# Kernel tuning notes

Measured on AMD Instinct MI355X. Metric: run time of the kernel, lower is better.

Reference implementation:

```python
import jax, jax.numpy as jnp
import numpy as np

NUM_HEADS = 8


def setup_inputs() -> dict:
    key = jax.random.key(0)
    ks = jax.random.split(key, 5)
    B, N, D = 2, 2048, 512
    scale = 1.0 / np.sqrt(D)  # xavier-ish init for stability
    return {
        "x": jax.random.normal(ks[0], (B, N, D), dtype=jnp.float32),
        "Wq": jax.random.normal(ks[1], (D, D), dtype=jnp.float32) * scale,
        "Wk": jax.random.normal(ks[2], (D, D), dtype=jnp.float32) * scale,
        "Wv": jax.random.normal(ks[3], (D, D), dtype=jnp.float32) * scale,
        "Wo": jax.random.normal(ks[4], (D, D), dtype=jnp.float32) * scale,
        "log_c": jnp.zeros((), dtype=jnp.float32),
        "log_beta": jnp.zeros((), dtype=jnp.float32),
    }


def reference(x, Wq, Wk, Wv, Wo, log_c, log_beta):
    B, N, D = x.shape
    H = NUM_HEADS
    dh = D // H

    # torch nn.Linear: y = x @ W.T
    def proj(W):
        return (x @ W.T).reshape(B, N, H, dh).transpose(0, 2, 1, 3)  # [B,H,N,dh]

    q, k, v = proj(Wq), proj(Wk), proj(Wv)

    c = jax.nn.softplus(log_c)
    beta = jax.nn.softplus(log_beta) + 0.5

    q_nsq = jnp.sum(q * q, axis=-1)  # [B,H,N]
    k_nsq = jnp.sum(k * k, axis=-1)  # [B,H,N]
    qk = jnp.einsum("bhnd,bhmd->bhnm", q, k)  # [B,H,N,N]

    diff_sq = jnp.maximum(q_nsq[..., :, None] - 2.0 * qk + k_nsq[..., None, :], 0.0)
    hyp_factor = jnp.sqrt(1.0 + c * (q_nsq[..., :, None] + k_nsq[..., None, :]))
    dist = jnp.sqrt(diff_sq + 1e-8) * hyp_factor
    scores = -beta * dist

    # causal mask (original: causal = mask is not None)
    causal = jnp.tril(jnp.ones((N, N), dtype=bool))
    scores = jnp.where(causal, scores, -jnp.inf)

    p = jax.nn.softmax(scores, axis=-1)
    out = jnp.einsum("bhnm,bhmd->bhnd", p, v)  # [B,H,N,dh]
    out = out.transpose(0, 2, 1, 3).reshape(B, N, D)
    return out @ Wo.T
```

## Files before the change

kernel.cpp:

```cpp
#include <hip/hip_runtime.h>
#include <math.h>

#define BB   2
#define NN   2048
#define DDIM 512
#define HH   8
#define DH   64
#define MTOT (BB*NN)
#define EE   (BB*HH*NN*DH)
#define CPB  144
#define NSLOT (BB*HH*CPB)

typedef __attribute__((ext_vector_type(8))) short bf16x8;
typedef __attribute__((ext_vector_type(4))) float f32x4;

__device__ __forceinline__ float softplus_f(float x) {
    return x > 20.f ? x : log1pf(expf(x));
}
__device__ __forceinline__ unsigned short f2bf(float x) {
    union { float f; unsigned u; } v; v.f = x;
    unsigned r = v.u + 0x7fffu + ((v.u >> 16) & 1u);
    return (unsigned short)(r >> 16);
}
__device__ __forceinline__ float bf2f(unsigned short h) {
    union { unsigned u; float f; } v; v.u = ((unsigned)h) << 16; return v.f;
}
__device__ __forceinline__ void split4(float4 v, ushort4& h, ushort4& l) {
    h.x = f2bf(v.x); l.x = f2bf(v.x - bf2f(h.x));
    h.y = f2bf(v.y); l.y = f2bf(v.y - bf2f(h.y));
    h.z = f2bf(v.z); l.z = f2bf(v.z - bf2f(h.z));
    h.w = f2bf(v.w); l.w = f2bf(v.w - bf2f(h.w));
}

__global__ __launch_bounds__(256, 3)
void mm_proj(const float* __restrict__ Xf,
             const float* __restrict__ W0, const float* __restrict__ W1,
             const float* __restrict__ W2,
             unsigned short* __restrict__ Qhi, unsigned short* __restrict__ Qlo,
             unsigned short* __restrict__ Khi, unsigned short* __restrict__ Klo,
             unsigned short* __restrict__ Vt,
             float* __restrict__ QN, float* __restrict__ KN)
{
    const int mode = blockIdx.z;
    const float* W = (mode == 1) ? W1 : ((mode == 2) ? W2 : W0);
    const int m0 = blockIdx.x * 64, n0 = blockIdx.y * 128;

    __shared__ unsigned short Ah_s[4 * 64 * 8];
    __shared__ unsigned short Al_s[4 * 64 * 8];
    __shared__ unsigned short Bh_s[4 * 128 * 8];
    __shared__ unsigned short Bl_s[4 * 128 * 8];

    const int tid  = threadIdx.x;
    const int lane = tid & 63, lx = lane & 15, q4 = lane >> 4;
    const int w = tid >> 6, wm = w & 1, wn = w >> 1;
    const int rowA = tid & 63, kqA = tid >> 6;
    const int rowB = tid & 127, kbB = tid >> 7;

    f32x4 acc[2][4];
    #pragma unroll
    for (int mt = 0; mt < 2; ++mt)
        #pragma unroll
        for (int nt = 0; nt < 4; ++nt)
            acc[mt][nt] = (f32x4){0.f, 0.f, 0.f, 0.f};

    const int am = m0 + rowA;
    const size_t brow = (size_t)(n0 + rowB) * DDIM;

    float4 fa0, fa1, fb0, fb1, fb2, fb3;
    {
        const float* ap = Xf + (size_t)am * DDIM + kqA * 8;
        fa0 = *(const float4*)(ap);
        fa1 = *(const float4*)(ap + 4);
        const int eb = kbB * 8;
        fb0 = *(const float4*)(W + brow + eb);
        fb1 = *(const float4*)(W + brow + eb + 4);
        fb2 = *(const float4*)(W + brow + eb + 16);
        fb3 = *(const float4*)(W + brow + eb + 20);
    }

    for (int k0 = 0; k0 < DDIM; k0 += 32) {
        __syncthreads();
        {
            ushort4 h0, l0, h1, l1;
            split4(fa0, h0, l0); split4(fa1, h1, l1);
            const int off = (kqA << 9) + (rowA << 3);
            *(ushort4*)&Ah_s[off]     = h0;  *(ushort4*)&Ah_s[off + 4] = h1;
            *(ushort4*)&Al_s[off]     = l0;  *(ushort4*)&Al_s[off + 4] = l1;
            split4(fb0, h0, l0); split4(fb1, h1, l1);
            const int offb = (kbB << 10) + (rowB << 3);
            *(ushort4*)&Bh_s[offb]     = h0;  *(ushort4*)&Bh_s[offb + 4] = h1;
            *(ushort4*)&Bl_s[offb]     = l0;  *(ushort4*)&Bl_s[offb + 4] = l1;
            split4(fb2, h0, l0); split4(fb3, h1, l1);
            const int offb2 = ((kbB + 2) << 10) + (rowB << 3);
            *(ushort4*)&Bh_s[offb2]     = h0;  *(ushort4*)&Bh_s[offb2 + 4] = h1;
            *(ushort4*)&Bl_s[offb2]     = l0;  *(ushort4*)&Bl_s[offb2 + 4] = l1;
        }
        __syncthreads();

        if (k0 + 32 < DDIM) {
            const float* ap = Xf + (size_t)am * DDIM + k0 + 32 + kqA * 8;
            fa0 = *(const float4*)(ap);
            fa1 = *(const float4*)(ap + 4);
            const int eb = k0 + 32 + kbB * 8;
            fb0 = *(const float4*)(W + brow + eb);
            fb1 = *(const float4*)(W + brow + eb + 4);
            fb2 = *(const float4*)(W + brow + eb + 16);
            fb3 = *(const float4*)(W + brow + eb + 20);
        }

        bf16x8 fah[2], fal[2], fbh[4], fbl[4];
        #pragma unroll
        for (int mt = 0; mt < 2; ++mt) {
            const int off = (q4 << 9) + ((wm * 32 + mt * 16 + lx) << 3);
            fah[mt] = *(const bf16x8*)&Ah_s[off];
            fal[mt] = *(const bf16x8*)&Al_s[off];
        }
        #pragma unroll
        for (int nt = 0; nt < 4; ++nt) {
            const int off = (q4 << 10) + ((wn * 64 + nt * 16 + lx) << 3);
            fbh[nt] = *(const bf16x8*)&Bh_s[off];
            fbl[nt] = *(const bf16x8*)&Bl_s[off];
        }
        #pragma unroll
        for (int mt = 0; mt < 2; ++mt)
            #pragma unroll
            for (int nt = 0; nt < 4; ++nt) {
                acc[mt][nt] = __builtin_amdgcn_mfma_f32_16x16x32_bf16(fah[mt], fbh[nt], acc[mt][nt], 0, 0, 0);
                acc[mt][nt] = __builtin_amdgcn_mfma_f32_16x16x32_bf16(fah[mt], fbl[nt], acc[mt][nt], 0, 0, 0);
                acc[mt][nt] = __builtin_amdgcn_mfma_f32_16x16x32_bf16(fal[mt], fbh[nt], acc[mt][nt], 0, 0, 0);
            }
    }

    if (mode == 0 || mode == 1) {
        float* Np = (mode == 0) ? QN : KN;
        const int head = (n0 + wn * 64) >> 6;
        #pragma unroll
        for (int mt = 0; mt < 2; ++mt)
            #pragma unroll
            for (int r = 0; r < 4; ++r) {
                float s = 0.f;
                #pragma unroll
                for (int nt = 0; nt < 4; ++nt) s = fmaf(acc[mt][nt][r], acc[mt][nt][r], s);
                s += __shfl_xor(s, 1);
                s += __shfl_xor(s, 2);
                s += __shfl_xor(s, 4);
                s += __shfl_xor(s, 8);
                if (lx == 0) {
                    const int m = m0 + wm * 32 + mt * 16 + q4 * 4 + r;
                    Np[(size_t)((m >> 11) * HH + head) * NN + (m & 2047)] = s;
                }
            }
    }

    if (mode == 2) {
        #pragma unroll
        for (int mt = 0; mt < 2; ++mt) {
            const int mb = m0 + wm * 32 + mt * 16 + q4 * 4;
            const int b = mb >> 11, nb = mb & 2047;
            #pragma unroll
            for (int nt = 0; nt < 4; ++nt) {
                const int j = n0 + wn * 64 + nt * 16 + lx;
                ushort4 pv = make_ushort4(f2bf(acc[mt][nt][0]), f2bf(acc[mt][nt][1]),
                                          f2bf(acc[mt][nt][2]), f2bf(acc[mt][nt][3]));
                *(ushort4*)(Vt + ((size_t)(b * HH + (j >> 6)) * 64 + (j & 63)) * NN + nb) = pv;
            }
        }
    } else {
        #pragma unroll
        for (int mt = 0; mt < 2; ++mt) {
            #pragma unroll
            for (int r = 0; r < 4; ++r) {
                const int m = m0 + wm * 32 + mt * 16 + q4 * 4 + r;
                const int b = m >> 11, n2 = m & 2047;
                #pragma unroll
                for (int nt = 0; nt < 4; ++nt) {
                    const int j = n0 + wn * 64 + nt * 16 + lx;
                    const float v = acc[mt][nt][r];
                    const size_t idx = (((size_t)(b * HH + (j >> 6)) * NN + n2) << 6) + (j & 63);
                    const unsigned short h = f2bf(v);
                    const unsigned short l = f2bf(v - bf2f(h));
                    if (mode == 0) { Qhi[idx] = h; Qlo[idx] = l; }
                    else           { Khi[idx] = h; Klo[idx] = l; }
                }
            }
        }
    }
}

__global__ __launch_bounds__(256, 4)
void mm_out(const unsigned short* __restrict__ AO, const float* __restrict__ Wo,
            float* __restrict__ Outp)
{
    const int m0 = blockIdx.x * 64, n0 = blockIdx.y * 64;

    __shared__ unsigned short Ah_s[4 * 64 * 8];
    __shared__ unsigned short Bh_s[4 * 64 * 8];

    const int tid  = threadIdx.x;
    const int lane = tid & 63, lx = lane & 15, q4 = lane >> 4;
    const int w = tid >> 6, wm = w & 1, wn = w >> 1;
    const int rowA = tid & 63, kqA = tid >> 6;

    f32x4 acc[2][2];
    #pragma unroll
    for (int mt = 0; mt < 2; ++mt)
        #pragma unroll
        for (int nt = 0; nt < 2; ++nt)
            acc[mt][nt] = (f32x4){0.f, 0.f, 0.f, 0.f};

    const int am = m0 + rowA;
    const int ab = am >> 11, an = am & 2047;
    const size_t brow = (size_t)(n0 + rowA) * DDIM;

    uint4 rah; float4 fb0, fb1;
    {
        const int e = kqA * 8;
        rah = *(const uint4*)(AO + (((size_t)(ab * HH + (e >> 6)) * NN + an) << 6) + (e & 63));
        fb0 = *(const float4*)(Wo + brow + e);
        fb1 = *(const float4*)(Wo + brow + e + 4);
    }

    for (int k0 = 0; k0 < DDIM; k0 += 32) {
        __syncthreads();
        {
            const int off = (kqA << 9) + (rowA << 3);
            *(uint4*)&Ah_s[off] = rah;
            ushort4 h0 = make_ushort4(f2bf(fb0.x), f2bf(fb0.y), f2bf(fb0.z), f2bf(fb0.w));
            ushort4 h1 = make_ushort4(f2bf(fb1.x), f2bf(fb1.y), f2bf(fb1.z), f2bf(fb1.w));
            *(ushort4*)&Bh_s[off]     = h0;
            *(ushort4*)&Bh_s[off + 4] = h1;
        }
        __syncthreads();

        if (k0 + 32 < DDIM) {
            const int e = k0 + 32 + kqA * 8;
            rah = *(const uint4*)(AO + (((size_t)(ab * HH + (e >> 6)) * NN + an) << 6) + (e & 63));
            fb0 = *(const float4*)(Wo + brow + e);
            fb1 = *(const float4*)(Wo + brow + e + 4);
        }

        bf16x8 fah[2], fbh[2];
        #pragma unroll
        for (int mt = 0; mt < 2; ++mt)
            fah[mt] = *(const bf16x8*)&Ah_s[(q4 << 9) + ((wm * 32 + mt * 16 + lx) << 3)];
        #pragma unroll
        for (int nt = 0; nt < 2; ++nt)
            fbh[nt] = *(const bf16x8*)&Bh_s[(q4 << 9) + ((wn * 32 + nt * 16 + lx) << 3)];
        #pragma unroll
        for (int mt = 0; mt < 2; ++mt)
            #pragma unroll
            for (int nt = 0; nt < 2; ++nt)
                acc[mt][nt] = __builtin_amdgcn_mfma_f32_16x16x32_bf16(fah[mt], fbh[nt], acc[mt][nt], 0, 0, 0);
    }

    #pragma unroll
    for (int mt = 0; mt < 2; ++mt)
        #pragma unroll
        for (int r = 0; r < 4; ++r) {
            const int m = m0 + wm * 32 + mt * 16 + q4 * 4 + r;
            #pragma unroll
            for (int nt = 0; nt < 2; ++nt)
                Outp[(size_t)m * DDIM + n0 + wn * 32 + nt * 16 + lx] = acc[mt][nt][r];
        }
}

__global__ __launch_bounds__(256, 4)
void attn_mfma(const unsigned short* __restrict__ Qhi, const unsigned short* __restrict__ Qlo,
               const unsigned short* __restrict__ Khi, const unsigned short* __restrict__ Klo,
               const unsigned short* __restrict__ Vt,
               const float* __restrict__ QN, const float* __restrict__ KN,
               const float* __restrict__ pLC, const float* __restrict__ pLB,
               float* __restrict__ Opart, float* __restrict__ Mp, float* __restrict__ Lp)
{
    __shared__ unsigned short Kh_s[8 * 64 * 8];
    __shared__ unsigned short Kl_s[8 * 64 * 8];
    __shared__ unsigned short Vt_s[8 * 64 * 8];
    __shared__ unsigned short P_s [8 * 64 * 8];
    __shared__ __align__(16) float kn_s[64];
    __shared__ float qn_s[64];

    const int idx = blockIdx.x;
    const int g   = (idx >= 112) ? 7 : (idx >= 84) ? 6 : (idx >= 60) ? 5 :
                    (idx >= 40) ? 4 : (idx >= 24) ? 3 : (idx >= 12) ? 2 :
                    (idx >= 4)  ? 1 : 0;
    const int rem = idx - 2 * g * (g + 1);
    const int C   = g + 1;
    const int qt  = g * 4 + rem / C;
    const int c0  = rem % C;
    const int bh  = blockIdx.y;
    const int nk  = qt + 1;
    const int kt0  = (c0 * nk) / C;
    const int kend = ((c0 + 1) * nk) / C;

    const int tid  = threadIdx.x;
    const int w    = tid >> 6;
    const int lane = tid & 63;
    const int lx   = lane & 15;
    const int q4   = lane >> 4;
    const int qrl  = w * 16 + lx;

    const float hc    = softplus_f(pLC[0]);
    const float betaL = (softplus_f(pLB[0]) + 0.5f) * 1.44269504f;

    const size_t base = ((size_t)bh * NN) << 6;

    const unsigned short* qrh = Qhi + base + ((size_t)(qt * 64 + qrl) << 6) + q4 * 8;
    const unsigned short* qrl_p = Qlo + base + ((size_t)(qt * 64 + qrl) << 6) + q4 * 8;
    const bf16x8 qh0 = *(const bf16x8*)(qrh);
    const bf16x8 qh1 = *(const bf16x8*)(qrh + 32);
    const bf16x8 ql0 = *(const bf16x8*)(qrl_p);
    const bf16x8 ql1 = *(const bf16x8*)(qrl_p + 32);

    if (tid < 64) qn_s[tid] = QN[(size_t)bh * NN + qt * 64 + tid];

    f32x4 Oacc[4];
    #pragma unroll
    for (int t = 0; t < 4; ++t) Oacc[t] = (f32x4){0.f, 0.f, 0.f, 0.f};
    float m_st = -INFINITY, l_st = 0.f;

    const int sc = tid >> 6, sr = tid & 63;

    uint4 pKh0, pKh1, pKl0, pKl1, pVt0, pVt1; float pkn = 0.f;
    {
        const unsigned short* kh = Khi + base + ((size_t)(kt0 * 64 + sr) << 6) + sc * 8;
        const unsigned short* kl = Klo + base + ((size_t)(kt0 * 64 + sr) << 6) + sc * 8;
        const unsigned short* vt = Vt  + base + (size_t)sr * NN + kt0 * 64 + sc * 8;
        pKh0 = *(const uint4*)(kh);  pKh1 = *(const uint4*)(kh + 32);
        pKl0 = *(const uint4*)(kl);  pKl1 = *(const uint4*)(kl + 32);
        pVt0 = *(const uint4*)(vt);  pVt1 = *(const uint4*)(vt + 32);
        if (tid < 64) pkn = KN[(size_t)bh * NN + kt0 * 64 + tid];
    }

    __syncthreads();
    const float qn = qn_s[qrl];

    for (int kt = kt0; kt < kend; ++kt) {
        const int soff = (sc << 9) + (sr << 3);
        *(uint4*)&Kh_s[soff]            = pKh0;
        *(uint4*)&Kh_s[soff + (4 << 9)] = pKh1;
        *(uint4*)&Kl_s[soff]            = pKl0;
        *(uint4*)&Kl_s[soff + (4 << 9)] = pKl1;
        *(uint4*)&Vt_s[soff]            = pVt0;
        *(uint4*)&Vt_s[soff + (4 << 9)] = pVt1;
        if (tid < 64) kn_s[tid] = pkn;
        __syncthreads();

        if (kt + 1 < kend) {
            const unsigned short* kh = Khi + base + ((size_t)((kt + 1) * 64 + sr) << 6) + sc * 8;
            const unsigned short* kl = Klo + base + ((size_t)((kt + 1) * 64 + sr) << 6) + sc * 8;
            const unsigned short* vt = Vt  + base + (size_t)sr * NN + (kt + 1) * 64 + sc * 8;
            pKh0 = *(const uint4*)(kh);  pKh1 = *(const uint4*)(kh + 32);
            pKl0 = *(const uint4*)(kl);  pKl1 = *(const uint4*)(kl + 32);
            pVt0 = *(const uint4*)(vt);  pVt1 = *(const uint4*)(vt + 32);
            if (tid < 64) pkn = KN[(size_t)bh * NN + (kt + 1) * 64 + tid];
        }

        f32x4 S[4];
        #pragma unroll
        for (int t = 0; t < 4; ++t) {
            f32x4 acc = (f32x4){0.f, 0.f, 0.f, 0.f};
            #pragma unroll
            for (int c2 = 0; c2 < 2; ++c2) {
                const int off = ((c2 * 4 + q4) << 9) + ((t * 16 + lx) << 3);
                const bf16x8 kh = *(const bf16x8*)&Kh_s[off];
                const bf16x8 kl = *(const bf16x8*)&Kl_s[off];
                const bf16x8 qh = c2 ? qh1 : qh0;
                const bf16x8 ql = c2 ? ql1 : ql0;
                acc = __builtin_amdgcn_mfma_f32_16x16x32_bf16(kh, qh, acc, 0, 0, 0);
                acc = __builtin_amdgcn_mfma_f32_16x16x32_bf16(kh, ql, acc, 0, 0, 0);
                acc = __builtin_amdgcn_mfma_f32_16x16x32_bf16(kl, qh, acc, 0, 0, 0);
            }
            S[t] = acc;
        }

        const bool diag = (kt == qt);
        float mloc = -INFINITY;
        #pragma unroll
        for (int t = 0; t < 4; ++t) {
            float kn4[4];
            *(float4*)kn4 = *(const float4*)&kn_s[t * 16 + q4 * 4];
            #pragma unroll
            for (int r = 0; r < 4; ++r) {
                const float sumn = qn + kn4[r];
                float diff = fmaxf(fmaf(-2.f, S[t][r], sumn), 0.f);
                float s = -betaL * sqrtf(fmaf(hc, sumn, 1.f) * (diff + 1e-8f));
                if (diag && (t * 16 + q4 * 4 + r) > qrl) s = -INFINITY;
                S[t][r] = s;
                mloc = fmaxf(mloc, s);
            }
        }
        mloc = fmaxf(mloc, __shfl_xor(mloc, 16));
        mloc = fmaxf(mloc, __shfl_xor(mloc, 32));
        const float mn = fmaxf(m_st, mloc);
        const float al = exp2f(m_st - mn);
        m_st = mn;

        float rs = 0.f;
        #pragma unroll
        for (int t = 0; t < 4; ++t) {
            const float p0 = exp2f(S[t][0] - mn);
            const float p1 = exp2f(S[t][1] - mn);
            const float p2 = exp2f(S[t][2] - mn);
            const float p3 = exp2f(S[t][3] - mn);
            rs += (p0 + p1) + (p2 + p3);
            ushort4 pk = make_ushort4(f2bf(p0), f2bf(p1), f2bf(p2), f2bf(p3));
            *(ushort4*)&P_s[((2 * t + (q4 >> 1)) << 9) + (qrl << 3) + ((q4 & 1) << 2)] = pk;
        }
        rs += __shfl_xor(rs, 16);
        rs += __shfl_xor(rs, 32);
        l_st = l_st * al + rs;
        #pragma unroll
        for (int t = 0; t < 4; ++t) {
            Oacc[t][0] *= al; Oacc[t][1] *= al;
            Oacc[t][2] *= al; Oacc[t][3] *= al;
        }

        __builtin_amdgcn_wave_barrier();

        #pragma unroll
        for (int c2 = 0; c2 < 2; ++c2) {
            const bf16x8 pb = *(const bf16x8*)&P_s[((c2 * 4 + q4) << 9) + (qrl << 3)];
            #pragma unroll
            for (int t2 = 0; t2 < 4; ++t2) {
                const bf16x8 va = *(const bf16x8*)&Vt_s[((c2 * 4 + q4) << 9) + ((t2 * 16 + lx) << 3)];
                Oacc[t2] = __builtin_amdgcn_mfma_f32_16x16x32_bf16(va, pb, Oacc[t2], 0, 0, 0);
            }
        }
        __syncthreads();
    }

    const int slot = bh * CPB + idx;
    float* op = Opart + ((size_t)slot << 12);
    #pragma unroll
    for (int t2 = 0; t2 < 4; ++t2)
        *(f32x4*)&op[qrl * 64 + t2 * 16 + q4 * 4] = Oacc[t2];
    if (q4 == 0) {
        Mp[slot * 64 + qrl] = m_st;
        Lp[slot * 64 + qrl] = l_st;
    }
}

__global__ __launch_bounds__(256)
void attn_combine(const float* __restrict__ Opart, const float* __restrict__ Mp,
                  const float* __restrict__ Lp, unsigned short* __restrict__ AO)
{
    const int bh = blockIdx.x >> 5, qt = blockIdx.x & 31;
    const int g = qt >> 2, C = g + 1;
    const int first = 2 * g * (g + 1) + (qt & 3) * C;
    const int row = threadIdx.x >> 2, qd = threadIdx.x & 3;
    const int slot0 = bh * CPB + first;

    float m = -INFINITY;
    for (int c = 0; c < C; ++c) m = fmaxf(m, Mp[(slot0 + c) * 64 + row]);
    float L = 0.f;
    float o[16];
    #pragma unroll
    for (int j = 0; j < 16; ++j) o[j] = 0.f;

    for (int c = 0; c < C; ++c) {
        const float wgt = exp2f(Mp[(slot0 + c) * 64 + row] - m);
        L += wgt * Lp[(slot0 + c) * 64 + row];
        const float* op = Opart + (((size_t)(slot0 + c)) << 12) + row * 64 + qd * 16;
        #pragma unroll
        for (int j4 = 0; j4 < 4; ++j4) {
            float4 v = *(const float4*)(op + j4 * 4);
            o[j4*4+0] = fmaf(wgt, v.x, o[j4*4+0]);
            o[j4*4+1] = fmaf(wgt, v.y, o[j4*4+1]);
            o[j4*4+2] = fmaf(wgt, v.z, o[j4*4+2]);
            o[j4*4+3] = fmaf(wgt, v.w, o[j4*4+3]);
        }
    }

    const float inv = 1.f / L;
    const size_t obase = (((size_t)bh * NN + qt * 64 + row) << 6) + qd * 16;
    union { unsigned short u[8]; uint4 v; } h2[2];
    #pragma unroll
    for (int j = 0; j < 16; ++j)
        h2[j >> 3].u[j & 7] = f2bf(o[j] * inv);
    *(uint4*)(AO + obase)     = h2[0].v;
    *(uint4*)(AO + obase + 8) = h2[1].v;
}

extern "C" void kernel_launch(void* const* d_in, const int* in_sizes, int n_in,
                              void* d_out, int out_size, void* d_ws, size_t ws_size,
                              hipStream_t stream)
{
    const float* x        = (const float*)d_in[0];
    const float* Wq       = (const float*)d_in[1];
    const float* Wk       = (const float*)d_in[2];
    const float* Wv       = (const float*)d_in[3];
    const float* Wo       = (const float*)d_in[4];
    const float* log_c    = (const float*)d_in[5];
    const float* log_beta = (const float*)d_in[6];
    float* out = (float*)d_out;

    unsigned short* p = (unsigned short*)d_ws;
    unsigned short* Qhi = p;            p += EE;
    unsigned short* Qlo = p;            p += EE;
    unsigned short* Khi = p;            p += EE;
    unsigned short* Klo = p;            p += EE;
    unsigned short* Vtr = p;            p += EE;
    unsigned short* AO  = p;            p += EE;
    float* QN    = (float*)p;
    float* KN    = QN + (size_t)BB * HH * NN;
    float* Opart = KN + (size_t)BB * HH * NN;
    float* Mp    = Opart + (size_t)NSLOT * 64 * 64;
    float* Lp    = Mp + (size_t)NSLOT * 64;

    mm_proj<<<dim3(MTOT / 64, DDIM / 128, 3), 256, 0, stream>>>(
        x, Wq, Wk, Wv, Qhi, Qlo, Khi, Klo, Vtr, QN, KN);
    attn_mfma<<<dim3(CPB, 16), 256, 0, stream>>>(Qhi, Qlo, Khi, Klo, Vtr, QN, KN,
                                                 log_c, log_beta, Opart, Mp, Lp);
    attn_combine<<<dim3(512), 256, 0, stream>>>(Opart, Mp, Lp, AO);
    mm_out<<<dim3(MTOT / 64, DDIM / 64), 256, 0, stream>>>(AO, Wo, out);
}
```

Before: 190.5 us.

## Pre-split weights to bf16, drop V split-precision MFMAs, store partials as bf16

Adds a split_w kernel that converts Wq/Wk/Wv into bf16 hi/lo pairs and Wo into bf16 once per call, so the GEMM kernels stop re-splitting fp32 weights in every block. The V projection (mode 2) now uses a single bf16 MFMA instead of three-term split precision. Attention partial outputs are written and read as bf16 rather than fp32, halving combine traffic. Conversions use hardware packed bf16 intrinsics. This adds an extra launch and lowers V and partial-output precision.

```diff
diff --git a/kernel.cpp b/kernel.cpp
--- a/kernel.cpp
+++ b/kernel.cpp
@@ -1,4 +1,5 @@
 #include <hip/hip_runtime.h>
+#include <hip/hip_bf16.h>
 #include <math.h>
 
 #define BB   2
@@ -8,6 +9,7 @@
 #define DH   64
 #define MTOT (BB*NN)
 #define EE   (BB*HH*NN*DH)
+#define WN   (DDIM*DDIM)
 #define CPB  144
 #define NSLOT (BB*HH*CPB)
 
@@ -31,18 +33,45 @@
     h.z = f2bf(v.z); l.z = f2bf(v.z - bf2f(h.z));
     h.w = f2bf(v.w); l.w = f2bf(v.w - bf2f(h.w));
 }
+__device__ __forceinline__ ushort4 pk4(float a, float b, float c, float d) {
+    union { __hip_bfloat162 b2[2]; ushort4 u4; } u;
+    u.b2[0] = __float22bfloat162_rn(make_float2(a, b));
+    u.b2[1] = __float22bfloat162_rn(make_float2(c, d));
+    return u.u4;
+}
+
+__global__ __launch_bounds__(256)
+void split_w(const float* __restrict__ Wq, const float* __restrict__ Wk,
+             const float* __restrict__ Wv, const float* __restrict__ Wo,
+             unsigned short* __restrict__ Whi, unsigned short* __restrict__ Wlo,
+             unsigned short* __restrict__ Wob)
+{
+    const int i = blockIdx.x * 256 + threadIdx.x;
+    const int y = blockIdx.y;
+    if (y < 3) {
+        const float* src = (y == 0) ? Wq : ((y == 1) ? Wk : Wv);
+        float4 v = *(const float4*)(src + 4 * (size_t)i);
+        ushort4 h, l;
+        split4(v, h, l);
+        *(ushort4*)(Whi + (size_t)y * WN + 4 * (size_t)i) = h;
+        *(ushort4*)(Wlo + (size_t)y * WN + 4 * (size_t)i) = l;
+    } else {
+        float4 v = *(const float4*)(Wo + 4 * (size_t)i);
+        *(ushort4*)(Wob + 4 * (size_t)i) = pk4(v.x, v.y, v.z, v.w);
+    }
+}
 
 __global__ __launch_bounds__(256, 3)
 void mm_proj(const float* __restrict__ Xf,
-             const float* __restrict__ W0, const float* __restrict__ W1,
-             const float* __restrict__ W2,
+             const unsigned short* __restrict__ Whi, const unsigned short* __restrict__ Wlo,
              unsigned short* __restrict__ Qhi, unsigned short* __restrict__ Qlo,
              unsigned short* __restrict__ Khi, unsigned short* __restrict__ Klo,
              unsigned short* __restrict__ Vt,
              float* __restrict__ QN, float* __restrict__ KN)
 {
     const int mode = blockIdx.z;
-    const float* W = (mode == 1) ? W1 : ((mode == 2) ? W2 : W0);
+    const unsigned short* Wh = Whi + (size_t)mode * WN;
+    const unsigned short* Wl = Wlo + (size_t)mode * WN;
     const int m0 = blockIdx.x * 64, n0 = blockIdx.y * 128;
 
     __shared__ unsigned short Ah_s[4 * 64 * 8];
@@ -66,16 +95,19 @@
     const int am = m0 + rowA;
     const size_t brow = (size_t)(n0 + rowB) * DDIM;
 
-    float4 fa0, fa1, fb0, fb1, fb2, fb3;
+    float4 fa0, fa1;
+    uint4 rbh0, rbh1, rbl0, rbl1;
     {
         const float* ap = Xf + (size_t)am * DDIM + kqA * 8;
         fa0 = *(const float4*)(ap);
         fa1 = *(const float4*)(ap + 4);
         const int eb = kbB * 8;
-        fb0 = *(const float4*)(W + brow + eb);
-        fb1 = *(const float4*)(W + brow + eb + 4);
-        fb2 = *(const float4*)(W + brow + eb + 16);
-        fb3 = *(const float4*)(W + brow + eb + 20);
+        rbh0 = *(const uint4*)(Wh + brow + eb);
+        rbh1 = *(const uint4*)(Wh + brow + eb + 16);
+        if (mode != 2) {
+            rbl0 = *(const uint4*)(Wl + brow + eb);
+            rbl1 = *(const uint4*)(Wl + brow + eb + 16);
+        }
     }
 
     for (int k0 = 0; k0 < DDIM; k0 += 32) {
@@ -85,15 +117,17 @@
             split4(fa0, h0, l0); split4(fa1, h1, l1);
             const int off = (kqA << 9) + (rowA << 3);
             *(ushort4*)&Ah_s[off]     = h0;  *(ushort4*)&Ah_s[off + 4] = h1;
-            *(ushort4*)&Al_s[off]     = l0;  *(ushort4*)&Al_s[off + 4] = l1;
-            split4(fb0, h0, l0); split4(fb1, h1, l1);
-            const int offb = (kbB << 10) + (rowB << 3);
-            *(ushort4*)&Bh_s[offb]     = h0;  *(ushort4*)&Bh_s[offb + 4] = h1;
-            *(ushort4*)&Bl_s[offb]     = l0;  *(ushort4*)&Bl_s[offb + 4] = l1;
-            split4(fb2, h0, l0); split4(fb3, h1, l1);
+            if (mode != 2) {
+                *(ushort4*)&Al_s[off]     = l0;  *(ushort4*)&Al_s[off + 4] = l1;
+            }
+            const int offb  = (kbB << 10) + (rowB << 3);
             const int offb2 = ((kbB + 2) << 10) + (rowB << 3);
-            *(ushort4*)&Bh_s[offb2]     = h0;  *(ushort4*)&Bh_s[offb2 + 4] = h1;
-            *(ushort4*)&Bl_s[offb2]     = l0;  *(ushort4*)&Bl_s[offb2 + 4] = l1;
+            *(uint4*)&Bh_s[offb]  = rbh0;
+            *(uint4*)&Bh_s[offb2] = rbh1;
+            if (mode != 2) {
+                *(uint4*)&Bl_s[offb]  = rbl0;
+                *(uint4*)&Bl_s[offb2] = rbl1;
+            }
         }
         __syncthreads();
 
@@ -102,10 +136,12 @@
             fa0 = *(const float4*)(ap);
             fa1 = *(const float4*)(ap + 4);
             const int eb = k0 + 32 + kbB * 8;
-            fb0 = *(const float4*)(W + brow + eb);
-            fb1 = *(const float4*)(W + brow + eb + 4);
-            fb2 = *(const float4*)(W + brow + eb + 16);
-            fb3 = *(const float4*)(W + brow + eb + 20);
+            rbh0 = *(const uint4*)(Wh + brow + eb);
+            rbh1 = *(const uint4*)(Wh + brow + eb + 16);
+            if (mode != 2) {
+                rbl0 = *(const uint4*)(Wl + brow + eb);
+                rbl1 = *(const uint4*)(Wl + brow + eb + 16);
+            }
         }
 
         bf16x8 fah[2], fal[2], fbh[4], fbl[4];
@@ -113,21 +149,23 @@
         for (int mt = 0; mt < 2; ++mt) {
             const int off = (q4 << 9) + ((wm * 32 + mt * 16 + lx) << 3);
             fah[mt] = *(const bf16x8*)&Ah_s[off];
-            fal[mt] = *(const bf16x8*)&Al_s[off];
+            if (mode != 2) fal[mt] = *(const bf16x8*)&Al_s[off];
         }
         #pragma unroll
         for (int nt = 0; nt < 4; ++nt) {
             const int off = (q4 << 10) + ((wn * 64 + nt * 16 + lx) << 3);
             fbh[nt] = *(const bf16x8*)&Bh_s[off];
-            fbl[nt] = *(const bf16x8*)&Bl_s[off];
+            if (mode != 2) fbl[nt] = *(const bf16x8*)&Bl_s[off];
         }
         #pragma unroll
         for (int mt = 0; mt < 2; ++mt)
             #pragma unroll
             for (int nt = 0; nt < 4; ++nt) {
                 acc[mt][nt] = __builtin_amdgcn_mfma_f32_16x16x32_bf16(fah[mt], fbh[nt], acc[mt][nt], 0, 0, 0);
-                acc[mt][nt] = __builtin_amdgcn_mfma_f32_16x16x32_bf16(fah[mt], fbl[nt], acc[mt][nt], 0, 0, 0);
-                acc[mt][nt] = __builtin_amdgcn_mfma_f32_16x16x32_bf16(fal[mt], fbh[nt], acc[mt][nt], 0, 0, 0);
+                if (mode != 2) {
+                    acc[mt][nt] = __builtin_amdgcn_mfma_f32_16x16x32_bf16(fah[mt], fbl[nt], acc[mt][nt], 0, 0, 0);
+                    acc[mt][nt] = __builtin_amdgcn_mfma_f32_16x16x32_bf16(fal[mt], fbh[nt], acc[mt][nt], 0, 0, 0);
+                }
             }
     }
 
@@ -160,8 +198,8 @@
             #pragma unroll
             for (int nt = 0; nt < 4; ++nt) {
                 const int j = n0 + wn * 64 + nt * 16 + lx;
-                ushort4 pv = make_ushort4(f2bf(acc[mt][nt][0]), f2bf(acc[mt][nt][1]),
-                                          f2bf(acc[mt][nt][2]), f2bf(acc[mt][nt][3]));
+                ushort4 pv = pk4(acc[mt][nt][0], acc[mt][nt][1],
+                                 acc[mt][nt][2], acc[mt][nt][3]);
                 *(ushort4*)(Vt + ((size_t)(b * HH + (j >> 6)) * 64 + (j & 63)) * NN + nb) = pv;
             }
         }
@@ -188,7 +226,7 @@
 }
 
 __global__ __launch_bounds__(256, 4)
-void mm_out(const unsigned short* __restrict__ AO, const float* __restrict__ Wo,
+void mm_out(const unsigned short* __restrict__ AO, const unsigned short* __restrict__ Wob,
             float* __restrict__ Outp)
 {
     const int m0 = blockIdx.x * 64, n0 = blockIdx.y * 64;
@@ -212,12 +250,11 @@
     const int ab = am >> 11, an = am & 2047;
     const size_t brow = (size_t)(n0 + rowA) * DDIM;
 
-    uint4 rah; float4 fb0, fb1;
+    uint4 rah, rbh;
     {
         const int e = kqA * 8;
         rah = *(const uint4*)(AO + (((size_t)(ab * HH + (e >> 6)) * NN + an) << 6) + (e & 63));
-        fb0 = *(const float4*)(Wo + brow + e);
-        fb1 = *(const float4*)(Wo + brow + e + 4);
+        rbh = *(const uint4*)(Wob + brow + e);
     }
 
     for (int k0 = 0; k0 < DDIM; k0 += 32) {
@@ -225,18 +262,14 @@
         {
             const int off = (kqA << 9) + (rowA << 3);
             *(uint4*)&Ah_s[off] = rah;
-            ushort4 h0 = make_ushort4(f2bf(fb0.x), f2bf(fb0.y), f2bf(fb0.z), f2bf(fb0.w));
-            ushort4 h1 = make_ushort4(f2bf(fb1.x), f2bf(fb1.y), f2bf(fb1.z), f2bf(fb1.w));
-            *(ushort4*)&Bh_s[off]     = h0;
-            *(ushort4*)&Bh_s[off + 4] = h1;
+            *(uint4*)&Bh_s[off] = rbh;
         }
         __syncthreads();
 
         if (k0 + 32 < DDIM) {
             const int e = k0 + 32 + kqA * 8;
             rah = *(const uint4*)(AO + (((size_t)(ab * HH + (e >> 6)) * NN + an) << 6) + (e & 63));
-            fb0 = *(const float4*)(Wo + brow + e);
-            fb1 = *(const float4*)(Wo + brow + e + 4);
+            rbh = *(const uint4*)(Wob + brow + e);
         }
 
         bf16x8 fah[2], fbh[2];
@@ -270,7 +303,7 @@
                const unsigned short* __restrict__ Vt,
                const float* __restrict__ QN, const float* __restrict__ KN,
                const float* __restrict__ pLC, const float* __restrict__ pLB,
-               float* __restrict__ Opart, float* __restrict__ Mp, float* __restrict__ Lp)
+               unsigned short* __restrict__ Opart, float* __restrict__ Mp, float* __restrict__ Lp)
 {
     __shared__ unsigned short Kh_s[8 * 64 * 8];
     __shared__ unsigned short Kl_s[8 * 64 * 8];
@@ -403,8 +436,8 @@
             const float p2 = exp2f(S[t][2] - mn);
             const float p3 = exp2f(S[t][3] - mn);
             rs += (p0 + p1) + (p2 + p3);
-            ushort4 pk = make_ushort4(f2bf(p0), f2bf(p1), f2bf(p2), f2bf(p3));
-            *(ushort4*)&P_s[((2 * t + (q4 >> 1)) << 9) + (qrl << 3) + ((q4 & 1) << 2)] = pk;
+            *(ushort4*)&P_s[((2 * t + (q4 >> 1)) << 9) + (qrl << 3) + ((q4 & 1) << 2)] =
+                pk4(p0, p1, p2, p3);
         }
         rs += __shfl_xor(rs, 16);
         rs += __shfl_xor(rs, 32);
@@ -430,10 +463,11 @@
     }
 
     const int slot = bh * CPB + idx;
-    float* op = Opart + ((size_t)slot << 12);
+    unsigned short* op = Opart + ((size_t)slot << 12);
     #pragma unroll
     for (int t2 = 0; t2 < 4; ++t2)
-        *(f32x4*)&op[qrl * 64 + t2 * 16 + q4 * 4] = Oacc[t2];
+        *(ushort4*)&op[qrl * 64 + t2 * 16 + q4 * 4] =
+            pk4(Oacc[t2][0], Oacc[t2][1], Oacc[t2][2], Oacc[t2][3]);
     if (q4 == 0) {
         Mp[slot * 64 + qrl] = m_st;
         Lp[slot * 64 + qrl] = l_st;
@@ -441,7 +475,7 @@
 }
 
 __global__ __launch_bounds__(256)
-void attn_combine(const float* __restrict__ Opart, const float* __restrict__ Mp,
+void attn_combine(const unsigned short* __restrict__ Opart, const float* __restrict__ Mp,
                   const float* __restrict__ Lp, unsigned short* __restrict__ AO)
 {
     const int bh = blockIdx.x >> 5, qt = blockIdx.x & 31;
@@ -460,25 +494,23 @@
     for (int c = 0; c < C; ++c) {
         const float wgt = exp2f(Mp[(slot0 + c) * 64 + row] - m);
         L += wgt * Lp[(slot0 + c) * 64 + row];
-        const float* op = Opart + (((size_t)(slot0 + c)) << 12) + row * 64 + qd * 16;
-        #pragma unroll
-        for (int j4 = 0; j4 < 4; ++j4) {
-            float4 v = *(const float4*)(op + j4 * 4);
-            o[j4*4+0] = fmaf(wgt, v.x, o[j4*4+0]);
-            o[j4*4+1] = fmaf(wgt, v.y, o[j4*4+1]);
-            o[j4*4+2] = fmaf(wgt, v.z, o[j4*4+2]);
-            o[j4*4+3] = fmaf(wgt, v.w, o[j4*4+3]);
+        const unsigned short* op = Opart + (((size_t)(slot0 + c)) << 12) + row * 64 + qd * 16;
+        union { uint4 v; unsigned short u[8]; } a0, a1;
+        a0.v = *(const uint4*)(op);
+        a1.v = *(const uint4*)(op + 8);
+        #pragma unroll
+        for (int j = 0; j < 8; ++j) {
+            o[j]     = fmaf(wgt, bf2f(a0.u[j]), o[j]);
+            o[j + 8] = fmaf(wgt, bf2f(a1.u[j]), o[j + 8]);
         }
     }
 
     const float inv = 1.f / L;
     const size_t obase = (((size_t)bh * NN + qt * 64 + row) << 6) + qd * 16;
-    union { unsigned short u[8]; uint4 v; } h2[2];
-    #pragma unroll
-    for (int j = 0; j < 16; ++j)
-        h2[j >> 3].u[j & 7] = f2bf(o[j] * inv);
-    *(uint4*)(AO + obase)     = h2[0].v;
-    *(uint4*)(AO + obase + 8) = h2[1].v;
+    *(ushort4*)(AO + obase)      = pk4(o[0]*inv,  o[1]*inv,  o[2]*inv,  o[3]*inv);
+    *(ushort4*)(AO + obase + 4)  = pk4(o[4]*inv,  o[5]*inv,  o[6]*inv,  o[7]*inv);
+    *(ushort4*)(AO + obase + 8)  = pk4(o[8]*inv,  o[9]*inv,  o[10]*inv, o[11]*inv);
+    *(ushort4*)(AO + obase + 12) = pk4(o[12]*inv, o[13]*inv, o[14]*inv, o[15]*inv);
 }
 
 extern "C" void kernel_launch(void* const* d_in, const int* in_sizes, int n_in,
@@ -501,16 +533,20 @@
     unsigned short* Klo = p;            p += EE;
     unsigned short* Vtr = p;            p += EE;
     unsigned short* AO  = p;            p += EE;
-    float* QN    = (float*)p;
-    float* KN    = QN + (size_t)BB * HH * NN;
-    float* Opart = KN + (size_t)BB * HH * NN;
-    float* Mp    = Opart + (size_t)NSLOT * 64 * 64;
-    float* Lp    = Mp + (size_t)NSLOT * 64;
-
+    unsigned short* Whi = p;            p += 3 * (size_t)WN;
+    unsigned short* Wlo = p;            p += 3 * (size_t)WN;
+    unsigned short* Wob = p;            p += WN;
+    unsigned short* Opart = p;          p += (size_t)NSLOT * 4096;
+    float* QN = (float*)p;
+    float* KN = QN + (size_t)BB * HH * NN;
+    float* Mp = KN + (size_t)BB * HH * NN;
+    float* Lp = Mp + (size_t)NSLOT * 64;
+
+    split_w<<<dim3(WN / 1024, 4), 256, 0, stream>>>(Wq, Wk, Wv, Wo, Whi, Wlo, Wob);
     mm_proj<<<dim3(MTOT / 64, DDIM / 128, 3), 256, 0, stream>>>(
-        x, Wq, Wk, Wv, Qhi, Qlo, Khi, Klo, Vtr, QN, KN);
+        x, Whi, Wlo, Qhi, Qlo, Khi, Klo, Vtr, QN, KN);
     attn_mfma<<<dim3(CPB, 16), 256, 0, stream>>>(Qhi, Qlo, Khi, Klo, Vtr, QN, KN,
                                                  log_c, log_beta, Opart, Mp, Lp);
     attn_combine<<<dim3(512), 256, 0, stream>>>(Opart, Mp, Lp, AO);
-    mm_out<<<dim3(MTOT / 64, DDIM / 64), 256, 0, stream>>>(AO, Wo, out);
-}
+    mm_out<<<dim3(MTOT / 64, DDIM / 64), 256, 0, stream>>>(AO, Wob, out);
+}
```

New measurement: 183.3 us. 3.8% less time.
